# Kernel tuning notes

Hardware: AMD Instinct MI355X
Metric: run time of the kernel (lower is better)

## Reference

```python
import jax, jax.numpy as jnp
import numpy as np

# Dims (match init_kwargs)
B, S, D = 2, 2048, 2048
H = 16
Q_LORA, KV_LORA = 768, 512
NOPE, ROPE, VD = 128, 64, 128
QHD = NOPE + ROPE  # 192


def setup_inputs() -> dict:
    key = jax.random.key(0)
    ks = jax.random.split(key, 7)
    w = lambda k, shape: (jax.random.normal(k, shape, jnp.float32) * 0.02)
    return {
        "x": jax.random.normal(ks[0], (B, S, D), jnp.float32),
        "position": jnp.broadcast_to(jnp.arange(S, dtype=jnp.int32), (B, S)),
        "mask": jnp.tril(jnp.ones((1, 1, S, S), jnp.int32)),  # causal
        "w_q_down": w(ks[1], (D, Q_LORA)),                 # (in, out) layout
        "w_q_up": w(ks[2], (Q_LORA, H * QHD)),
        "w_kv_down": w(ks[3], (D, KV_LORA + ROPE)),
        "w_kv_up": w(ks[4], (KV_LORA, H * (NOPE + VD))),
        "w_out": w(ks[5], (H * VD, D)),
    }


def reference(x, position, mask, w_q_down, w_q_up, w_kv_down, w_kv_up, w_out):
    # position unused: rope_embedding is None in the source module.
    # Low-rank Q: down then up projection.
    q = (x @ w_q_down) @ w_q_up                      # [B,S,H*QHD]
    q = q.reshape(B, S, H, QHD).transpose(0, 2, 1, 3)  # [B,H,S,QHD]
    q_nope, q_rope = q[..., :NOPE], q[..., NOPE:]

    # Low-rank KV: down projection yields compressed kv + shared rope key.
    c = x @ w_kv_down                                # [B,S,KV_LORA+ROPE]
    c_kv, k_rope = c[..., :KV_LORA], c[..., KV_LORA:]
    k_rope = k_rope[:, None, :, :]                   # [B,1,S,ROPE]

    kv = (c_kv @ w_kv_up).reshape(B, S, H, NOPE + VD).transpose(0, 2, 1, 3)
    k_nope, v = kv[..., :NOPE], kv[..., NOPE:]       # [B,H,S,NOPE], [B,H,S,VD]

    q_state = jnp.concatenate([q_nope, q_rope], axis=-1)           # [B,H,S,QHD]
    k_state = jnp.concatenate(
        [k_nope, jnp.broadcast_to(k_rope, (B, H, S, ROPE))], axis=-1)

    scale = 1.0 / jnp.sqrt(jnp.float32(VD))  # source divides by sqrt(v_head_dim)
    scores = jnp.einsum("bhqd,bhkd->bhqk", q_state, k_state) * scale
    scores = jnp.where(mask == 0, jnp.float32(-jnp.inf), scores)
    att = jax.nn.softmax(scores, axis=-1)            # dropout_rate=0 (eval)
    out = jnp.einsum("bhqk,bhkd->bhqd", att, v)      # [B,H,S,VD]
    out = out.transpose(0, 2, 1, 3).reshape(B, S, H * VD)
    return out @ w_out
```

## Files before the change

### kernel.cpp

```cpp
#include <hip/hip_runtime.h>

typedef __bf16 bf16;
typedef bf16 bf16x8 __attribute__((ext_vector_type(8)));
typedef bf16 bf16x4 __attribute__((ext_vector_type(4)));
typedef float f32x4 __attribute__((ext_vector_type(4)));
typedef short s16x4 __attribute__((ext_vector_type(4)));

#define AS1 __attribute__((address_space(1)))
#define AS3 __attribute__((address_space(3)))

__device__ __forceinline__ void load_lds16(const void* g, void* l) {
    __builtin_amdgcn_global_load_lds((const AS1 unsigned int*)g,
                                     (AS3 unsigned int*)l, 16, 0, 0);
}

__device__ __forceinline__ void tc_body(
        const float* __restrict__ in, bf16* __restrict__ out,
        int K, int N, int Np, int bx, int by, int tid,
        float (*tile)[33]) {
    const int tx = tid & 31, ty = tid >> 5;
#pragma unroll
    for (int i = 0; i < 4; ++i) {
        int k = by + ty + i * 8, n = bx + tx;
        float v = (k < K && n < N) ? in[(size_t)k * N + n] : 0.f;
        tile[ty + i * 8][tx] = v;
    }
    __syncthreads();
#pragma unroll
    for (int i = 0; i < 4; ++i) {
        int n = bx + ty + i * 8, k = by + tx;
        if (n < Np && k < K) out[(size_t)n * K + k] = (bf16)tile[tx][ty + i * 8];
    }
}

__global__ __launch_bounds__(256) void prep_fused(
        const float* __restrict__ x,    bf16* __restrict__ xb,
        const float* __restrict__ wqd,  bf16* __restrict__ wqdT,
        const float* __restrict__ wkvd, bf16* __restrict__ wkvdT,
        const float* __restrict__ wqu,  bf16* __restrict__ wquT,
        const float* __restrict__ wkvu, bf16* __restrict__ wkvuT,
        const float* __restrict__ wout, bf16* __restrict__ woutT) {
    __shared__ float tile[32][33];
    const int tid = threadIdx.x;
    int r = blockIdx.x;
    if (r < 8192) {
        int i = (r * 256 + tid) * 4;
        float4 v = *(const float4*)(x + i);
        bf16x4 o = { (bf16)v.x, (bf16)v.y, (bf16)v.z, (bf16)v.w };
        *(bf16x4*)(xb + i) = o;
        return;
    }
    r -= 8192;
    if (r < 1536) { tc_body(wqd,  wqdT,  2048, 768,  768,  (r % 24) * 32, (r / 24) * 32, tid, tile); return; }
    r -= 1536;
    if (r < 1280) { tc_body(wkvd, wkvdT, 2048, 576,  640,  (r % 20) * 32, (r / 20) * 32, tid, tile); return; }
    r -= 1280;
    if (r < 2304) { tc_body(wqu,  wquT,  768,  3072, 3072, (r % 96) * 32, (r / 96) * 32, tid, tile); return; }
    r -= 2304;
    if (r < 2048) { tc_body(wkvu, wkvuT, 512,  4096, 4096, (r % 128) * 32, (r / 128) * 32, tid, tile); return; }
    r -= 2048;
    tc_body(wout, woutT, 2048, 2048, 2048, (r % 64) * 32, (r / 64) * 32, tid, tile);
}

__device__ __forceinline__ void gemm_acc(
        const bf16* __restrict__ A, const bf16* __restrict__ Bt,
        int K, int lda, int ldb, int m0, int n0,
        bf16* As, bf16* Bs, f32x4 acc[4][4]) {
    const int tid = threadIdx.x;
    const int wave = tid >> 6, lane = tid & 63;
    const int l15 = lane & 15, quad = lane >> 4;
    const int wm = (wave >> 1) * 64, wn = (wave & 1) * 64;

    for (int k0 = 0; k0 < K; k0 += 64) {
#pragma unroll
        for (int c = 0; c < 4; ++c) {
            int e = wave * 2048 + c * 512 + lane * 8;
            int r = e >> 6, col = e & 63;
            load_lds16(A + (size_t)(m0 + r) * lda + k0 + col,
                       &As[wave * 2048 + c * 512]);
            load_lds16(Bt + (size_t)(n0 + r) * ldb + k0 + col,
                       &Bs[wave * 2048 + c * 512]);
        }
        __syncthreads();
#pragma unroll
        for (int kk = 0; kk < 64; kk += 32) {
            bf16x8 af[4], bf[4];
#pragma unroll
            for (int i = 0; i < 4; ++i)
                af[i] = *(const bf16x8*)&As[(wm + i * 16 + l15) * 64 + kk + quad * 8];
#pragma unroll
            for (int j = 0; j < 4; ++j)
                bf[j] = *(const bf16x8*)&Bs[(wn + j * 16 + l15) * 64 + kk + quad * 8];
#pragma unroll
            for (int i = 0; i < 4; ++i)
#pragma unroll
                for (int j = 0; j < 4; ++j)
                    acc[i][j] = __builtin_amdgcn_mfma_f32_16x16x32_bf16(
                        af[i], bf[j], acc[i][j], 0, 0, 0);
        }
        __syncthreads();
    }
}

template <typename OutT>
__device__ __forceinline__ void store_c(
        f32x4 acc[4][4], OutT* __restrict__ C, int ldc, int m0, int n0) {
    const int tid = threadIdx.x;
    const int wave = tid >> 6, lane = tid & 63;
    const int l15 = lane & 15, quad = lane >> 4;
    const int wm = (wave >> 1) * 64, wn = (wave & 1) * 64;
#pragma unroll
    for (int i = 0; i < 4; ++i)
#pragma unroll
        for (int j = 0; j < 4; ++j) {
            int row = m0 + wm + i * 16 + quad * 4;
            int col = n0 + wn + j * 16 + l15;
#pragma unroll
            for (int r = 0; r < 4; ++r)
                C[(size_t)(row + r) * ldc + col] = (OutT)acc[i][j][r];
        }
}

template <typename OutT>
__global__ __launch_bounds__(256) void gemm_bt(
        const bf16* __restrict__ A, const bf16* __restrict__ Bt,
        OutT* __restrict__ C, int K, int lda, int ldb, int ldc) {
    __shared__ __align__(16) bf16 As[128 * 64];
    __shared__ __align__(16) bf16 Bs[128 * 64];
    f32x4 acc[4][4] = {};
    gemm_acc(A, Bt, K, lda, ldb, blockIdx.y * 128, blockIdx.x * 128, As, Bs, acc);
    store_c<OutT>(acc, C, ldc, blockIdx.y * 128, blockIdx.x * 128);
}

__global__ __launch_bounds__(256) void gemm_down(
        const bf16* __restrict__ A, const bf16* __restrict__ Bt,
        bf16* __restrict__ C1, bf16* __restrict__ C2) {
    __shared__ __align__(16) bf16 As[128 * 64];
    __shared__ __align__(16) bf16 Bs[128 * 64];
    f32x4 acc[4][4] = {};
    const int n0 = blockIdx.x * 128, m0 = blockIdx.y * 128;
    gemm_acc(A, Bt, 2048, 2048, 2048, m0, n0, As, Bs, acc);
    if (n0 < 768) store_c<bf16>(acc, C1, 768, m0, n0);
    else          store_c<bf16>(acc, C2, 640, m0, n0 - 768);
}

__global__ __launch_bounds__(512, 2) void gemm_up256(
        const bf16* __restrict__ qd, const bf16* __restrict__ wquT,
        bf16* __restrict__ qb,
        const bf16* __restrict__ cb, const bf16* __restrict__ wkvuT,
        bf16* __restrict__ kvb, bf16* __restrict__ vtb) {
    __shared__ __align__(16) bf16 sh[65536];
    const int tid = threadIdx.x;
    const int wave = tid >> 6, lane = tid & 63;
    const int l15 = lane & 15, quad = lane >> 4;
    const int wr = wave >> 2, wc = wave & 3;
    const int m0 = blockIdx.y * 256;
    const bool is_q = blockIdx.x < 12;
    const int n0 = is_q ? blockIdx.x * 256 : (blockIdx.x - 12) * 256;
    const bf16* Ag  = is_q ? qd : cb;
    const bf16* Btg = is_q ? wquT : wkvuT;
    const int lda = is_q ? 768 : 640;
    const int ldb = is_q ? 768 : 512;
    const int NT  = is_q ? 12 : 8;

    const int gcol = (((tid & 7) ^ ((tid >> 3) & 7)) * 8);
    auto stage = [&](int kt, int bufi) {
        const int k0 = kt * 64;
#pragma unroll
        for (int c = 0; c < 4; ++c) {
            const int row = c * 64 + (tid >> 3);
            const int ldsb = bufi * 16384 + c * 4096 + wave * 512;
            load_lds16(Ag  + (size_t)(m0 + row) * lda + k0 + gcol, &sh[ldsb]);
            load_lds16(Btg + (size_t)(n0 + row) * ldb + k0 + gcol, &sh[32768 + ldsb]);
        }
    };

    const int sw = (l15 & 7) * 8;
    f32x4 acc[8][4] = {};

    stage(0, 0);
    asm volatile("s_waitcnt vmcnt(0)" ::: "memory");
    __builtin_amdgcn_s_barrier();
    __builtin_amdgcn_sched_barrier(0);

    for (int kt = 0; kt < NT; ++kt) {
        const int bufi = kt & 1;
        const bf16* As_ = &sh[bufi * 16384];
        const bf16* Bs_ = &sh[32768 + bufi * 16384];
        bf16x8 bfr[4][2];
#pragma unroll
        for (int p = 0; p < 4; ++p) {
            bf16x8 afr[2][2];
#pragma unroll
            for (int ii = 0; ii < 2; ++ii) {
                const int arow = (wr * 128 + (p * 2 + ii) * 16 + l15) * 64;
#pragma unroll
                for (int kki = 0; kki < 2; ++kki)
                    afr[ii][kki] = *(const bf16x8*)&As_[arow + ((kki * 32 + quad * 8) ^ sw)];
            }
            if (p == 0) {
#pragma unroll
                for (int j = 0; j < 4; ++j) {
                    const int brow = (wc * 64 + j * 16 + l15) * 64;
#pragma unroll
                    for (int kki = 0; kki < 2; ++kki)
                        bfr[j][kki] = *(const bf16x8*)&Bs_[brow + ((kki * 32 + quad * 8) ^ sw)];
                }
                if (kt + 1 < NT) stage(kt + 1, bufi ^ 1);
            }
            __builtin_amdgcn_s_barrier();
            asm volatile("s_waitcnt lgkmcnt(0)" ::: "memory");
            __builtin_amdgcn_sched_barrier(0);
            __builtin_amdgcn_s_setprio(1);
#pragma unroll
            for (int ii = 0; ii < 2; ++ii)
#pragma unroll
                for (int j = 0; j < 4; ++j)
#pragma unroll
                    for (int kki = 0; kki < 2; ++kki)
                        acc[p * 2 + ii][j] = __builtin_amdgcn_mfma_f32_16x16x32_bf16(
                            afr[ii][kki], bfr[j][kki], acc[p * 2 + ii][j], 0, 0, 0);
            __builtin_amdgcn_s_setprio(0);
            if (p == 3) asm volatile("s_waitcnt vmcnt(0)" ::: "memory");
            __builtin_amdgcn_s_barrier();
            __builtin_amdgcn_sched_barrier(0);
        }
    }

    if (is_q) {
#pragma unroll
        for (int i = 0; i < 8; ++i)
#pragma unroll
            for (int j = 0; j < 4; ++j) {
                const int row = m0 + wr * 128 + i * 16 + quad * 4;
                const int col = n0 + wc * 64 + j * 16 + l15;
#pragma unroll
                for (int r = 0; r < 4; ++r)
                    qb[(size_t)(row + r) * 3072 + col] = (bf16)acc[i][j][r];
            }
        return;
    }
    const int h = n0 >> 8;
    const int bb = m0 >> 11, kvbase = m0 & 2047;
    bf16* t = sh;
    if (wc < 2) {
#pragma unroll
        for (int i = 0; i < 8; ++i)
#pragma unroll
            for (int j = 0; j < 4; ++j) {
                const int row = m0 + wr * 128 + i * 16 + quad * 4;
                const int col = h * 256 + wc * 64 + j * 16 + l15;
#pragma unroll
                for (int r = 0; r < 4; ++r)
                    kvb[(size_t)(row + r) * 4096 + col] = (bf16)acc[i][j][r];
            }
    } else {
#pragma unroll
        for (int i = 0; i < 8; ++i)
#pragma unroll
            for (int j = 0; j < 4; ++j) {
                const int vd = (wc - 2) * 64 + j * 16 + l15;
                const int kv = wr * 128 + i * 16 + quad * 4;
                bf16x4 v;
#pragma unroll
                for (int r = 0; r < 4; ++r) v[r] = (bf16)acc[i][j][r];
                *(bf16x4*)&t[vd * 264 + kv] = v;
            }
    }
    __syncthreads();
    {
        bf16* vt = vtb + (size_t)((bb * 16 + h) * 128) * 2048;
        const int vd = tid >> 2;
        const int kv4 = (tid & 3) * 64;
#pragma unroll
        for (int u = 0; u < 8; ++u) {
            bf16x8 vv = *(const bf16x8*)&t[vd * 264 + kv4 + u * 8];
            *(bf16x8*)&vt[(size_t)vd * 2048 + kvbase + kv4 + u * 8] = vv;
        }
    }
}

__global__ __launch_bounds__(1024, 4) void mla_attention_split(
        const bf16* __restrict__ qb, const bf16* __restrict__ kvb,
        const bf16* __restrict__ cb, const bf16* __restrict__ vtb,
        bf16* __restrict__ ob, bf16* __restrict__ part_o,
        float* __restrict__ part_ml) {
    constexpr int S = 2048;
    const signed char k_of[20]  = {7,7,7,7, 6,6,6,6, 5,5,5, 4,4,4, 3,3, 2,2, 1, 0};
    const signed char c_of[20]  = {0,1,2,3, 0,1,2,3, 0,1,2, 0,1,2, 0,1, 0,1, 0, 0};
    const signed char np_of[8]  = {1,1,2,2,3,3,4,4};
    const signed char pre_of[8] = {0,0,0,1,2,4,6,9};

    const int k  = k_of[blockIdx.x], c = c_of[blockIdx.x];
    const int np = np_of[k];
    const int h = blockIdx.y, b = blockIdx.z;
    const int T  = 4 * k + 4;
    const int t0 = (c * T) / np, t1 = ((c + 1) * T) / np;
    const int q0 = k * 256;

    const int tid = threadIdx.x, wave = tid >> 6, lane = tid & 63;
    const int l15 = lane & 15, quad = lane >> 4;

    __shared__ __align__(16) bf16 Ks[2][24 * 512];
    __shared__ __align__(16) bf16 Vs[2][8 * 1024];

    const int qrow = q0 + wave * 16 + l15;
    bf16x8 qf[6];
    {
        const bf16* qr = qb + (size_t)(b * S + qrow) * 3072 + h * 192;
#pragma unroll
        for (int ks = 0; ks < 6; ++ks)
            qf[ks] = *(const bf16x8*)(qr + ks * 32 + quad * 8);
    }

    const bf16* vt_head = vtb + (size_t)((b * 16 + h) * 128) * 2048;

    auto stage = [&](int kt, int bufi) {
        const int kv0 = kt * 64;
        if (wave < 8) {
            const int mt = wave >> 1;
            const size_t row = (size_t)(b * S + kv0 + mt * 16 + l15);
#pragma unroll
            for (int i = 0; i < 3; ++i) {
                const int ks = (wave & 1) * 3 + i;
                const bf16* g = (ks < 4)
                    ? kvb + row * 4096 + h * 256 + ks * 32 + quad * 8
                    : cb  + row * 640  + 512 + (ks - 4) * 32 + quad * 8;
                load_lds16(g, &Ks[bufi][(mt * 6 + ks) * 512]);
            }
        } else {
            const int nt = wave - 8;
#pragma unroll
            for (int i = 0; i < 2; ++i) {
                const bf16* g = vt_head + (size_t)(nt * 16 + l15) * 2048
                                + kv0 + (i * 4 + quad) * 8;
                load_lds16(g, &Vs[bufi][nt * 1024 + i * 512]);
            }
        }
    };

    f32x4 o[8] = {};
    float m_i = -1e30f, l_i = 0.f;
    const float sm_scale = 0.08838834764831845f * 1.4426950408889634f;
    const int qmin_w = q0 + wave * 16;

    stage(t0, 0);
    stage(t0 + 1, 1);

    int cur = 0;
    for (int kt = t0; kt < t1; ++kt, cur ^= 1) {
        const int kv0 = kt * 64;

        if (kt + 1 < t1) {
            if (wave < 8) asm volatile("s_waitcnt vmcnt(3)" ::: "memory");
            else          asm volatile("s_waitcnt vmcnt(2)" ::: "memory");
        } else {
            asm volatile("s_waitcnt vmcnt(0)" ::: "memory");
        }
        __builtin_amdgcn_s_barrier();
        __builtin_amdgcn_sched_barrier(0);

        f32x4 s[4];
        __builtin_amdgcn_s_setprio(1);
#pragma unroll
        for (int mt = 0; mt < 4; ++mt) {
            f32x4 a = {};
#pragma unroll
            for (int ks = 0; ks < 6; ++ks) {
                bf16x8 kf = *(const bf16x8*)&Ks[cur][(mt * 6 + ks) * 512 + lane * 8];
                a = __builtin_amdgcn_mfma_f32_16x16x32_bf16(kf, qf[ks], a, 0, 0, 0);
            }
            s[mt] = a;
        }
        __builtin_amdgcn_s_setprio(0);

        if (kv0 + 63 > qmin_w) {
#pragma unroll
            for (int mt = 0; mt < 4; ++mt)
#pragma unroll
                for (int r = 0; r < 4; ++r) {
                    int kvi = kv0 + mt * 16 + quad * 4 + r;
                    s[mt][r] = (kvi <= qrow) ? s[mt][r] * sm_scale : -1e30f;
                }
        } else {
#pragma unroll
            for (int mt = 0; mt < 4; ++mt)
#pragma unroll
                for (int r = 0; r < 4; ++r)
                    s[mt][r] = s[mt][r] * sm_scale;
        }
        float mx4[4];
#pragma unroll
        for (int mt = 0; mt < 4; ++mt)
            mx4[mt] = fmaxf(fmaxf(s[mt][0], s[mt][1]),
                            fmaxf(s[mt][2], s[mt][3]));
        float mx = fmaxf(fmaxf(mx4[0], mx4[1]), fmaxf(mx4[2], mx4[3]));
        mx = fmaxf(mx, __shfl_xor(mx, 16, 64));
        mx = fmaxf(mx, __shfl_xor(mx, 32, 64));
        float m_new = fmaxf(m_i, mx);
        float su4[4];
        bf16x4 pf[4];
#pragma unroll
        for (int mt = 0; mt < 4; ++mt) {
            float e0 = exp2f(s[mt][0] - m_new);
            float e1 = exp2f(s[mt][1] - m_new);
            float e2 = exp2f(s[mt][2] - m_new);
            float e3 = exp2f(s[mt][3] - m_new);
            su4[mt] = (e0 + e1) + (e2 + e3);
            pf[mt][0] = (bf16)e0; pf[mt][1] = (bf16)e1;
            pf[mt][2] = (bf16)e2; pf[mt][3] = (bf16)e3;
        }
        float su = (su4[0] + su4[1]) + (su4[2] + su4[3]);
        su += __shfl_xor(su, 16, 64);
        su += __shfl_xor(su, 32, 64);
        if (__all(mx <= m_i)) {
            l_i += su;
        } else {
            float alpha = exp2f(m_i - m_new);
            l_i = l_i * alpha + su;
            m_i = m_new;
            float alpha_r[4];
#pragma unroll
            for (int r = 0; r < 4; ++r)
                alpha_r[r] = __shfl(alpha, quad * 4 + r, 64);
#pragma unroll
            for (int nt = 0; nt < 8; ++nt)
#pragma unroll
                for (int r = 0; r < 4; ++r) o[nt][r] *= alpha_r[r];
        }

        __builtin_amdgcn_s_setprio(1);
#pragma unroll
        for (int ktk = 0; ktk < 4; ++ktk) {
            s16x4 a = __builtin_bit_cast(s16x4, pf[ktk]);
            const int voff = ktk * 256 + (quad >> 1) * 128 + l15 * 8 + (quad & 1) * 4;
#pragma unroll
            for (int nt = 0; nt < 8; ++nt) {
                s16x4 bfv = __builtin_bit_cast(s16x4,
                    *(const bf16x4*)&Vs[cur][nt * 1024 + voff]);
                o[nt] = __builtin_amdgcn_mfma_f32_16x16x16bf16_1k(a, bfv, o[nt], 0, 0, 0);
            }
        }
        __builtin_amdgcn_s_setprio(0);

        __builtin_amdgcn_s_barrier();
        if (kt + 2 < t1) stage(kt + 2, cur);
    }

    if (np == 1) {
        float l_r[4];
#pragma unroll
        for (int r = 0; r < 4; ++r) l_r[r] = __shfl(l_i, quad * 4 + r, 64);
        bf16* obase = ob + (size_t)(b * S + q0 + wave * 16) * 2048 + h * 128;
#pragma unroll
        for (int nt = 0; nt < 8; ++nt)
#pragma unroll
            for (int r = 0; r < 4; ++r)
                obase[(size_t)(quad * 4 + r) * 2048 + nt * 16 + l15] =
                    (bf16)(o[nt][r] / l_r[r]);
    } else {
        const int bh = b * 16 + h;
        if (quad == 0) {
            const int qlocal = wave * 16 + l15;
            float* mlp = part_ml + ((size_t)(bh * 8 + k) * 4 + c) * 512;
            mlp[qlocal] = m_i;
            mlp[256 + qlocal] = l_i;
        }
        if (c == np - 1) {
            bf16* obase = ob + (size_t)(b * S + q0 + wave * 16) * 2048 + h * 128;
#pragma unroll
            for (int nt = 0; nt < 8; ++nt)
#pragma unroll
                for (int r = 0; r < 4; ++r)
                    obase[(size_t)(quad * 4 + r) * 2048 + nt * 16 + l15] =
                        (bf16)o[nt][r];
        } else {
            bf16* pb = part_o + (size_t)(bh * 12 + pre_of[k] + c) * 32768
                       + (size_t)(wave * 16) * 128;
#pragma unroll
            for (int nt = 0; nt < 8; ++nt)
#pragma unroll
                for (int r = 0; r < 4; ++r)
                    pb[(quad * 4 + r) * 128 + nt * 16 + l15] = (bf16)o[nt][r];
        }
    }
}

__global__ __launch_bounds__(256) void mla_merge(
        const bf16* __restrict__ part_o, const float* __restrict__ part_ml,
        bf16* __restrict__ ob) {
    const signed char np_of[8]  = {1,1,2,2,3,3,4,4};
    const signed char pre_of[8] = {0,0,0,1,2,4,6,9};
    const int k = 2 + blockIdx.x;
    const int h = blockIdx.y, b = blockIdx.z;
    const int bh = b * 16 + h;
    const int np = np_of[k];
    const int row = threadIdx.x;

    const float* mlb = part_ml + (size_t)(bh * 8 + k) * 4 * 512;
    const float m0 = mlb[row],            l0 = mlb[256 + row];
    const float m1 = mlb[512 + row],      l1 = mlb[512 + 256 + row];
    const float m2 = (np > 2) ? mlb[1024 + row] : -1e30f;
    const float l2 = (np > 2) ? mlb[1024 + 256 + row] : 0.f;
    const float m3 = (np > 3) ? mlb[1536 + row] : -1e30f;
    const float l3 = (np > 3) ? mlb[1536 + 256 + row] : 0.f;
    const float M = fmaxf(fmaxf(m0, m1), fmaxf(m2, m3));
    float a0 = exp2f(m0 - M), a1 = exp2f(m1 - M);
    float a2 = exp2f(m2 - M), a3 = exp2f(m3 - M);
    const float inv = 1.f / (l0 * a0 + l1 * a1 + l2 * a2 + l3 * a3);
    a0 *= inv; a1 *= inv; a2 *= inv; a3 *= inv;
    const float alast = (np == 2) ? a1 : (np == 3) ? a2 : a3;

    const bf16* p0 = part_o + (size_t)(bh * 12 + pre_of[k]) * 32768 + row * 128;
    const bf16* p1 = p0 + 32768;
    const bf16* p2 = p1 + 32768;
    bf16* po = ob + (size_t)(b * 2048 + k * 256 + row) * 2048 + h * 128;
#pragma unroll
    for (int i = 0; i < 16; ++i) {
        bf16x8 vb = *(const bf16x8*)(po + i * 8);
        bf16x8 v0 = *(const bf16x8*)(p0 + i * 8);
        float acc[8];
#pragma unroll
        for (int u = 0; u < 8; ++u)
            acc[u] = (float)vb[u] * alast + (float)v0[u] * a0;
        if (np > 2) {
            bf16x8 v1 = *(const bf16x8*)(p1 + i * 8);
#pragma unroll
            for (int u = 0; u < 8; ++u) acc[u] += (float)v1[u] * a1;
        }
        if (np > 3) {
            bf16x8 v2 = *(const bf16x8*)(p2 + i * 8);
#pragma unroll
            for (int u = 0; u < 8; ++u) acc[u] += (float)v2[u] * a2;
        }
        bf16x8 om;
#pragma unroll
        for (int u = 0; u < 8; ++u) om[u] = (bf16)acc[u];
        *(bf16x8*)(po + i * 8) = om;
    }
}

extern "C" void kernel_launch(void* const* d_in, const int* in_sizes, int n_in,
                              void* d_out, int out_size, void* d_ws, size_t ws_size,
                              hipStream_t stream) {
    const float* x    = (const float*)d_in[0];
    const float* wqd  = (const float*)d_in[3];
    const float* wqu  = (const float*)d_in[4];
    const float* wkvd = (const float*)d_in[5];
    const float* wkvu = (const float*)d_in[6];
    const float* wout = (const float*)d_in[7];
    float* out = (float*)d_out;
    char* ws = (char*)d_ws;

    bf16* xb    = (bf16*)(ws + 0);
    bf16* vtb   = (bf16*)(ws + 0);
    bf16* wqdT  = (bf16*)(ws + 16777216);
    bf16* wkvdT = (bf16*)(ws + 19922944);
    bf16* wquT  = (bf16*)(ws + 22544384);
    bf16* wkvuT = (bf16*)(ws + 27262976);
    float* part_ml = (float*)(ws + 16777216);
    bf16* part_o  = (bf16*)out;
    bf16* woutT = (bf16*)(ws + 31457280);
    bf16* qd    = (bf16*)(ws + 39845888);
    bf16* qb    = (bf16*)(ws + 46137344);
    bf16* cb    = (bf16*)(ws + 71303168);
    bf16* kvb   = (bf16*)(ws + 76546048);
    bf16* attnb = (bf16*)(ws + 110100480);

    prep_fused<<<19456, 256, 0, stream>>>(x, xb, wqd, wqdT, wkvd, wkvdT,
                                          wqu, wquT, wkvu, wkvuT, wout, woutT);

    gemm_down<<<dim3(11, 32), 256, 0, stream>>>(xb, wqdT, qd, cb);
    gemm_up256<<<dim3(28, 16), 512, 0, stream>>>(qd, wquT, qb, cb, wkvuT, kvb, vtb);

    mla_attention_split<<<dim3(20, 16, 2), 1024, 0, stream>>>(
        qb, kvb, cb, vtb, attnb, part_o, part_ml);
    mla_merge<<<dim3(6, 16, 2), 256, 0, stream>>>(part_o, part_ml, attnb);

    gemm_bt<float><<<dim3(16, 32), 256, 0, stream>>>(attnb, woutT, out, 2048, 2048, 2048, 2048);
}
```

Measured before the change: 442.0 us.

## Replace output projection GEMM with 256x128-tile double-buffered pipelined kernel

Swaps the generic 128x128 output-projection GEMM for a dedicated kernel using 256x128 tiles with 8 waves, double-buffered LDS filled by direct global-to-LDS loads, XOR-swizzled LDS layout, and per-subtile barriers with raised wave priority around MFMA. The aim is to overlap the global loads for the next K tile with MFMA compute and to improve operand reuse, cutting memory stalls in the final 4096x2048x2048 GEMM. It halves the grid to 256 blocks, which may underfill the CUs, and uses 96KB of LDS per block.

```diff
diff --git a/kernel.cpp b/kernel.cpp
--- a/kernel.cpp
+++ b/kernel.cpp
@@ -119,17 +119,6 @@
             for (int r = 0; r < 4; ++r)
                 C[(size_t)(row + r) * ldc + col] = (OutT)acc[i][j][r];
         }
-}
-
-template <typename OutT>
-__global__ __launch_bounds__(256) void gemm_bt(
-        const bf16* __restrict__ A, const bf16* __restrict__ Bt,
-        OutT* __restrict__ C, int K, int lda, int ldb, int ldc) {
-    __shared__ __align__(16) bf16 As[128 * 64];
-    __shared__ __align__(16) bf16 Bs[128 * 64];
-    f32x4 acc[4][4] = {};
-    gemm_acc(A, Bt, K, lda, ldb, blockIdx.y * 128, blockIdx.x * 128, As, Bs, acc);
-    store_c<OutT>(acc, C, ldc, blockIdx.y * 128, blockIdx.x * 128);
 }
 
 __global__ __launch_bounds__(256) void gemm_down(
@@ -280,6 +269,95 @@
     }
 }
 
+__global__ __launch_bounds__(512, 2) void gemm_out256(
+        const bf16* __restrict__ A, const bf16* __restrict__ Bt,
+        float* __restrict__ C) {
+    __shared__ __align__(16) bf16 sh[49152];
+    const int tid = threadIdx.x;
+    const int wave = tid >> 6, lane = tid & 63;
+    const int l15 = lane & 15, quad = lane >> 4;
+    const int wr = wave >> 1, wc = wave & 1;
+    const int m0 = blockIdx.y * 256, n0 = blockIdx.x * 128;
+    const int NT = 32;
+
+    const int gcol = (((tid & 7) ^ ((tid >> 3) & 7)) * 8);
+    auto stage = [&](int kt, int bufi) {
+        const int k0 = kt * 64;
+#pragma unroll
+        for (int c = 0; c < 4; ++c) {
+            const int row = c * 64 + (tid >> 3);
+            load_lds16(A + (size_t)(m0 + row) * 2048 + k0 + gcol,
+                       &sh[bufi * 16384 + c * 4096 + wave * 512]);
+        }
+#pragma unroll
+        for (int c = 0; c < 2; ++c) {
+            const int row = c * 64 + (tid >> 3);
+            load_lds16(Bt + (size_t)(n0 + row) * 2048 + k0 + gcol,
+                       &sh[32768 + bufi * 8192 + c * 4096 + wave * 512]);
+        }
+    };
+
+    const int sw = (l15 & 7) * 8;
+    f32x4 acc[4][4] = {};
+
+    stage(0, 0);
+    asm volatile("s_waitcnt vmcnt(0)" ::: "memory");
+    __builtin_amdgcn_s_barrier();
+    __builtin_amdgcn_sched_barrier(0);
+
+    for (int kt = 0; kt < NT; ++kt) {
+        const int bufi = kt & 1;
+        const bf16* As_ = &sh[bufi * 16384];
+        const bf16* Bs_ = &sh[32768 + bufi * 8192];
+        bf16x8 bfr[4][2];
+#pragma unroll
+        for (int p = 0; p < 4; ++p) {
+            bf16x8 afr[2];
+            {
+                const int arow = (wr * 64 + p * 16 + l15) * 64;
+#pragma unroll
+                for (int kki = 0; kki < 2; ++kki)
+                    afr[kki] = *(const bf16x8*)&As_[arow + ((kki * 32 + quad * 8) ^ sw)];
+            }
+            if (p == 0) {
+#pragma unroll
+                for (int j = 0; j < 4; ++j) {
+                    const int brow = (wc * 64 + j * 16 + l15) * 64;
+#pragma unroll
+                    for (int kki = 0; kki < 2; ++kki)
+                        bfr[j][kki] = *(const bf16x8*)&Bs_[brow + ((kki * 32 + quad * 8) ^ sw)];
+                }
+                if (kt + 1 < NT) stage(kt + 1, bufi ^ 1);
+            }
+            __builtin_amdgcn_s_barrier();
+            asm volatile("s_waitcnt lgkmcnt(0)" ::: "memory");
+            __builtin_amdgcn_sched_barrier(0);
+            __builtin_amdgcn_s_setprio(1);
+#pragma unroll
+            for (int j = 0; j < 4; ++j)
+#pragma unroll
+                for (int kki = 0; kki < 2; ++kki)
+                    acc[p][j] = __builtin_amdgcn_mfma_f32_16x16x32_bf16(
+                        afr[kki], bfr[j][kki], acc[p][j], 0, 0, 0);
+            __builtin_amdgcn_s_setprio(0);
+            if (p == 3) asm volatile("s_waitcnt vmcnt(0)" ::: "memory");
+            __builtin_amdgcn_s_barrier();
+            __builtin_amdgcn_sched_barrier(0);
+        }
+    }
+
+#pragma unroll
+    for (int i = 0; i < 4; ++i)
+#pragma unroll
+        for (int j = 0; j < 4; ++j) {
+            const int row = m0 + wr * 64 + i * 16 + quad * 4;
+            const int col = n0 + wc * 64 + j * 16 + l15;
+#pragma unroll
+            for (int r = 0; r < 4; ++r)
+                C[(size_t)(row + r) * 2048 + col] = acc[i][j][r];
+        }
+}
+
 __global__ __launch_bounds__(1024, 4) void mla_attention_split(
         const bf16* __restrict__ qb, const bf16* __restrict__ kvb,
         const bf16* __restrict__ cb, const bf16* __restrict__ vtb,
@@ -577,5 +655,5 @@
         qb, kvb, cb, vtb, attnb, part_o, part_ml);
     mla_merge<<<dim3(6, 16, 2), 256, 0, stream>>>(part_o, part_ml, attnb);
 
-    gemm_bt<float><<<dim3(16, 32), 256, 0, stream>>>(attnb, woutT, out, 2048, 2048, 2048, 2048);
-}
+    gemm_out256<<<dim3(16, 16), 512, 0, stream>>>(attnb, woutT, out);
+}
```

Measured after the change: 434.8 us. About the same (-1.6%).
